# Kernel optimization log

Hardware: AMD Instinct MI355X
Metric: run time of the kernel (lower is better)

Reference implementation:

```python
import jax, jax.numpy as jnp
import numpy as np

H_PATCH, W_PATCH = 14, 14
NUM_HEADS, HEAD_DIM = 12, 64


def _relative_position_index(h, w):
    ch, cw = np.meshgrid(np.arange(h), np.arange(w), indexing='ij')
    coords = np.stack([ch.ravel(), cw.ravel()])          # (2, h*w)
    rel = coords[:, :, None] - coords[:, None, :]        # (2, L, L)
    rel = rel.transpose(1, 2, 0)
    rel[:, :, 0] += h - 1
    rel[:, :, 1] += w - 1
    rel[:, :, 0] *= 2 * w - 1
    return rel.sum(-1)                                    # (h*w, h*w) int


def setup_inputs() -> dict:
    key = jax.random.key(0)
    ks = jax.random.split(key, 16)
    B, L, C = 256, 197, 768
    s = 0.02
    return {
        'hidden_states': jax.random.normal(ks[0], (B, L, C), jnp.float32),
        'Wq': jax.random.normal(ks[1], (C, C), jnp.float32) * s,
        'bq': jax.random.normal(ks[2], (C,), jnp.float32) * s,
        'Wk': jax.random.normal(ks[3], (C, C), jnp.float32) * s,
        'bk': jax.random.normal(ks[4], (C,), jnp.float32) * s,
        'Wv': jax.random.normal(ks[5], (C, C), jnp.float32) * s,
        'bv': jax.random.normal(ks[6], (C,), jnp.float32) * s,
        'Wo': jax.random.normal(ks[7], (C, C), jnp.float32) * s,
        'bo': jax.random.normal(ks[8], (C,), jnp.float32) * s,
        'rel_table': jax.random.normal(ks[9], ((2 * H_PATCH - 1) * (2 * W_PATCH - 1), NUM_HEADS), jnp.float32) * s,
        'cls_to_patches': jax.random.normal(ks[10], (1, NUM_HEADS, 1, H_PATCH * W_PATCH), jnp.float32) * s,
        'patches_to_cls': jax.random.normal(ks[11], (1, NUM_HEADS, H_PATCH * W_PATCH, 1), jnp.float32) * s,
        'cls_to_cls': jax.random.normal(ks[12], (1, NUM_HEADS, 1, 1), jnp.float32) * s,
    }


def _full_bias(rel_table, cls_to_patches, patches_to_cls, cls_to_cls):
    idx = jnp.asarray(_relative_position_index(H_PATCH, W_PATCH))  # (P, P)
    patch_bias = rel_table[idx]                                    # (P, P, H)
    patch_bias = jnp.transpose(patch_bias, (2, 0, 1))[None]        # (1, H, P, P)
    top = jnp.concatenate([cls_to_cls, cls_to_patches], axis=-1)   # (1, H, 1, P+1)
    bottom = jnp.concatenate([patches_to_cls, patch_bias], axis=-1)
    return jnp.concatenate([top, bottom], axis=-2)                 # (1, H, L, L)


def reference(hidden_states, Wq, bq, Wk, bk, Wv, bv, Wo, bo,
              rel_table, cls_to_patches, patches_to_cls, cls_to_cls):
    B, L, C = hidden_states.shape
    Hh, D = NUM_HEADS, HEAD_DIM
    scale = D ** -0.5

    def heads(x, W, b):
        return (x @ W + b).reshape(B, L, Hh, D).transpose(0, 2, 1, 3)  # (B,H,L,D)

    q = heads(hidden_states, Wq, bq)
    k = heads(hidden_states, Wk, bk)
    v = heads(hidden_states, Wv, bv)

    attn = jnp.einsum('bhqd,bhkd->bhqk', q, k) * scale
    attn = attn + _full_bias(rel_table, cls_to_patches, patches_to_cls, cls_to_cls)
    attn = jax.nn.softmax(attn, axis=-1)

    x = jnp.einsum('bhqk,bhkd->bhqd', attn, v)            # (B,H,L,D)
    x = x.transpose(0, 2, 1, 3).reshape(B, L, C)
    return x @ Wo + bo
```

## Files before the change

kernel.cpp:

```cpp
#include <hip/hip_runtime.h>
#include <hip/hip_bf16.h>
#include <stdint.h>

#define LSEQ 197
#define NH   12
#define HD   64
#define CDIM 768
#define QKVS 2304

#define VSTRD 200

typedef __bf16 bf16x8 __attribute__((ext_vector_type(8)));
typedef float  f32x4  __attribute__((ext_vector_type(4)));
typedef unsigned short u16x4 __attribute__((ext_vector_type(4)));

__device__ __forceinline__ float bf2f(unsigned short u) { return __uint_as_float(((unsigned)u) << 16); }
__device__ __forceinline__ unsigned short f2bf(float f) {
  unsigned u = __float_as_uint(f);
  unsigned r = 0x7fffu + ((u >> 16) & 1u);
  return (unsigned short)((u + r) >> 16);
}

__device__ __forceinline__ void gload16(const void* g, void* l) {
  __builtin_amdgcn_global_load_lds(
      (const __attribute__((address_space(1))) unsigned int*)(g),
      (__attribute__((address_space(3))) unsigned int*)(l), 16, 0, 0);
}

__device__ __forceinline__ bf16x8 pack4(unsigned x, unsigned y, unsigned z, unsigned w) {
  union { unsigned u[4]; bf16x8 v; } t;
  t.u[0] = x; t.u[1] = y; t.u[2] = z; t.u[3] = w;
  return t.v;
}

__global__ void detect_dtype(const unsigned* __restrict__ x, int* __restrict__ flag) {
  __shared__ int cnt;
  if (threadIdx.x == 0) cnt = 0;
  __syncthreads();
  int local = 0;
  for (int i = threadIdx.x; i < 1024; i += 256) {
    const unsigned e = (x[i] >> 7) & 0xFFu;
    if (e >= 96u && e <= 140u) local++;
  }
  atomicAdd(&cnt, local);
  __syncthreads();
  if (threadIdx.x == 0) *flag = (cnt > 512) ? 0 : 1;
}

__global__ void convert_to_bf16(const void* __restrict__ in,
                                unsigned short* __restrict__ outb,
                                const int* __restrict__ flag, long n) {
  const long stride = (long)gridDim.x * blockDim.x;
  long i = (long)blockIdx.x * blockDim.x + threadIdx.x;
  if (*flag) {
    const float* f = (const float*)in;
    for (; i < n; i += stride) outb[i] = f2bf(f[i]);
  } else {
    const unsigned short* s = (const unsigned short*)in;
    for (; i < n; i += stride) outb[i] = s[i];
  }
}

__global__ void convert_small(const void* b0, const void* b1, const void* b2, const void* b3,
                              const void* r, const void* cp, const void* pc, const void* cc,
                              unsigned short* __restrict__ out, const int* __restrict__ flag) {
  const int starts[9] = {0, 768, 1536, 2304, 3072, 11820, 14172, 16524, 16536};
  const void* srcs[8] = {b0, b1, b2, b3, r, cp, pc, cc};
  const bool isf = (*flag != 0);
  for (int i = blockIdx.x * blockDim.x + threadIdx.x; i < 16536;
       i += gridDim.x * blockDim.x) {
    int seg = 0;
    while (i >= starts[seg + 1]) seg++;
    const int off = i - starts[seg];
    out[i] = isf ? f2bf(((const float*)srcs[seg])[off])
                 : ((const unsigned short*)srcs[seg])[off];
  }
}

__global__ void bias_build(const unsigned short* __restrict__ sm,
                           unsigned short* __restrict__ biasB) {
  const int gid = blockIdx.x * blockDim.x + threadIdx.x;
  if (gid >= 12 * 13 * 13 * 256) return;
  const int r    = gid & 3;
  const int lane = (gid >> 2) & 63;
  const int t    = gid >> 8;
  const int nt   = t % 13;
  const int mt   = (t / 13) % 13;
  const int h    = t / 169;
  const int q = mt * 16 + (lane & 15);
  const int k = nt * 16 + ((lane >> 4) & 3) * 4 + r;
  float v;
  if (q >= 197 || k >= 197) {
    v = -1e30f;
  } else {
    const unsigned short* rel = sm + 3072;
    const unsigned short* c2p = sm + 11820;
    const unsigned short* p2c = sm + 14172;
    const unsigned short* c2c = sm + 16524;
    unsigned short u;
    if (q == 0) {
      u = (k == 0) ? c2c[h] : c2p[h * 196 + (k - 1)];
    } else if (k == 0) {
      u = p2c[h * 196 + (q - 1)];
    } else {
      const int pi = q - 1, pj = k - 1;
      const int dh = pi / 14 - pj / 14 + 13;
      const int dw = pi % 14 - pj % 14 + 13;
      u = rel[(dh * 27 + dw) * 12 + h];
    }
    v = bf2f(u) * 1.4426950408889634f;
  }
  biasB[gid] = f2bf(v);
}

__global__ void transpose768_cvt(const void* __restrict__ in,
                                 unsigned short* __restrict__ out,
                                 const int* __restrict__ flag) {
  __shared__ unsigned short tile[32][33];
  const bool isf = (*flag != 0);
  const int tx = threadIdx.x & 31;
  const int ty = threadIdx.x >> 5;
  const int bx = blockIdx.x, by = blockIdx.y;
#pragma unroll
  for (int j = 0; j < 32; j += 8) {
    const size_t idx = (size_t)(by * 32 + ty + j) * CDIM + bx * 32 + tx;
    tile[ty + j][tx] = isf ? f2bf(((const float*)in)[idx])
                           : ((const unsigned short*)in)[idx];
  }
  __syncthreads();
#pragma unroll
  for (int j = 0; j < 32; j += 8)
    out[(size_t)(bx * 32 + ty + j) * CDIM + by * 32 + tx] = tile[tx][ty + j];
}

__global__ __launch_bounds__(256, 2) void gemm_bt_bias(
    const unsigned short* __restrict__ A,
    const unsigned short* __restrict__ Bt,
    const unsigned short* __restrict__ bias,
    void* __restrict__ C,
    int M, int N, int K,
    const int* __restrict__ outf32) {
  __shared__ unsigned short As[128 * 32];
  __shared__ unsigned short Bs[128 * 32];

  const int tid  = threadIdx.x;
  const int lane = tid & 63;
  const int wid  = tid >> 6;
  const int nwg = gridDim.x;
  const int q8 = nwg >> 3, r8 = nwg & 7;
  const int xcd = blockIdx.x & 7, ii = blockIdx.x >> 3;
  const int wg = (xcd < r8 ? xcd * (q8 + 1) : r8 * (q8 + 1) + (xcd - r8) * q8) + ii;
  const int nbn = N >> 7;
  const int bm = wg / nbn, bn = wg % nbn;
  const int wm = wid >> 1, wn = wid & 1;
  const bool wf32 = (outf32 != nullptr) && (*outf32 != 0);

  const int srow = (wid * 2) * 16 + (lane >> 2);
  const int scol = (lane & 3) * 8;
  const unsigned short* Ag = A  + (size_t)(bm * 128 + srow) * K + scol;
  const unsigned short* Bg = Bt + (size_t)(bn * 128 + srow) * K + scol;
  unsigned short* lA0 = &As[(wid * 2) * 16 * 32];
  unsigned short* lA1 = lA0 + 16 * 32;
  unsigned short* lB0 = &Bs[(wid * 2) * 16 * 32];
  unsigned short* lB1 = lB0 + 16 * 32;

  f32x4 acc[4][4] = {};

  for (int kt = 0; kt < K; kt += 32) {
    gload16(Ag, lA0);
    gload16(Ag + (size_t)16 * K, lA1);
    gload16(Bg, lB0);
    gload16(Bg + (size_t)16 * K, lB1);
    Ag += 32; Bg += 32;
    __syncthreads();

    bf16x8 fa[4], fb[4];
#pragma unroll
    for (int t = 0; t < 4; ++t) {
      fa[t] = *(const bf16x8*)&As[(wm * 64 + t * 16 + (lane & 15)) * 32 + (lane >> 4) * 8];
      fb[t] = *(const bf16x8*)&Bs[(wn * 64 + t * 16 + (lane & 15)) * 32 + (lane >> 4) * 8];
    }
#pragma unroll
    for (int mt = 0; mt < 4; ++mt)
#pragma unroll
      for (int nt = 0; nt < 4; ++nt)
        acc[mt][nt] = __builtin_amdgcn_mfma_f32_16x16x32_bf16(fa[mt], fb[nt], acc[mt][nt], 0, 0, 0);
    __syncthreads();
  }

  float bvv[4];
#pragma unroll
  for (int nt = 0; nt < 4; ++nt)
    bvv[nt] = bf2f(bias[bn * 128 + wn * 64 + nt * 16 + (lane & 15)]);

#pragma unroll
  for (int mt = 0; mt < 4; ++mt) {
    const int row0 = bm * 128 + wm * 64 + mt * 16 + (lane >> 4) * 4;
#pragma unroll
    for (int r = 0; r < 4; ++r) {
      const size_t rowoff = (size_t)(row0 + r) * N + bn * 128 + wn * 64 + (lane & 15);
#pragma unroll
      for (int nt = 0; nt < 4; ++nt) {
        const float val = acc[mt][nt][r] + bvv[nt];
        const size_t idx = rowoff + nt * 16;
        if (wf32) ((float*)C)[idx] = val;
        else      ((unsigned short*)C)[idx] = f2bf(val);
      }
    }
  }
}

__global__ __launch_bounds__(256, 3) void attn_mfma(
    const unsigned short* __restrict__ QKV,
    const unsigned short* __restrict__ biasB,
    unsigned short* __restrict__ ctx) {
  __shared__ unsigned short Kh[208 * 64];
  __shared__ unsigned short Vt[64 * VSTRD];

  const int tid  = threadIdx.x;
  const int lane = tid & 63;
  const int wid  = tid >> 6;
  const int bh = blockIdx.x;
  const int b = bh / NH;
  const int h = bh - b * NH;
  const size_t baseQ = (size_t)b * LSEQ * QKVS + (size_t)h * HD;
  const size_t baseK = baseQ + 768;
  const size_t baseV = baseQ + 1536;
  const size_t baseC = (size_t)b * LSEQ * CDIM + (size_t)h * HD;

  for (int i = tid; i < 197 * 8; i += 256) {
    const int l = i >> 3, c8 = (i & 7) * 8;
    const bf16x8 kv = *(const bf16x8*)&QKV[baseK + (size_t)l * QKVS + c8];
    *(bf16x8*)((char*)Kh + l * 128 + ((c8 * 2) ^ ((l & 7) << 4))) = kv;
  }
  for (int i = tid; i < 197 * 32; i += 256) {
    const int l = i >> 5, d2 = (i & 31) * 2;
    const unsigned vv = *(const unsigned*)&QKV[baseV + (size_t)l * QKVS + d2];
    Vt[d2 * VSTRD + l]       = (unsigned short)(vv & 0xffffu);
    Vt[(d2 + 1) * VSTRD + l] = (unsigned short)(vv >> 16);
  }
  for (int i = tid; i < 64 * 3; i += 256)
    Vt[(i / 3) * VSTRD + 197 + (i % 3)] = 0;
  __syncthreads();

  const int ql = lane & 15, g = lane >> 4;
  const int krd0 = ql * 128 + ((g * 16) ^ ((ql & 7) << 4));
  const int krd1 = ql * 128 + ((g * 16 + 64) ^ ((ql & 7) << 4));
  const int vrd  = ql * VSTRD + g * 8;
  const int vrd6 = ql * VSTRD + 192;
  const int addrA = (((g & 1) << 5) + ql) << 2;
  const int addrB = addrA + 64;
  const bool hi2 = lane >= 32;
  const bool hi1 = lane >= 16;

  for (int mt = wid; mt < 13; mt += 4) {
    const int qm = mt * 16 + ql;
    const unsigned short* qp =
        &QKV[baseQ + (size_t)(qm > 196 ? 196 : qm) * QKVS + g * 8];
    const bf16x8 qf0 = *(const bf16x8*)qp;
    const bf16x8 qf1 = *(const bf16x8*)(qp + 32);

    const unsigned short* bp =
        biasB + (size_t)(h * 13 + mt) * 13 * 256 + (lane << 2);
    u16x4 bq[13];
#pragma unroll
    for (int nt = 0; nt < 13; ++nt) bq[nt] = *(const u16x4*)(bp + nt * 256);

    f32x4 s[13];
#pragma unroll
    for (int nt = 0; nt < 13; ++nt) {
      const bf16x8 kb0 = *(const bf16x8*)((const char*)Kh + nt * 2048 + krd0);
      const bf16x8 kb1 = *(const bf16x8*)((const char*)Kh + nt * 2048 + krd1);
      f32x4 a = {0.f, 0.f, 0.f, 0.f};
      a = __builtin_amdgcn_mfma_f32_16x16x32_bf16(kb0, qf0, a, 0, 0, 0);
      a = __builtin_amdgcn_mfma_f32_16x16x32_bf16(kb1, qf1, a, 0, 0, 0);
      s[nt] = a;
    }

#pragma unroll
    for (int nt = 0; nt < 13; ++nt)
#pragma unroll
      for (int r = 0; r < 4; ++r)
        s[nt][r] = s[nt][r] * 0.18033688011112042f + bf2f(bq[nt][r]);

    const float NEG = -1e30f;
    s[12][0] = hi2 ? NEG : s[12][0];
    s[12][1] = hi1 ? NEG : s[12][1];
    s[12][2] = hi1 ? NEG : s[12][2];
    s[12][3] = hi1 ? NEG : s[12][3];

    float m0 = s[0][0], m1 = s[0][1], m2 = s[0][2], m3 = s[0][3];
#pragma unroll
    for (int nt = 1; nt < 13; ++nt) {
      m0 = fmaxf(m0, s[nt][0]); m1 = fmaxf(m1, s[nt][1]);
      m2 = fmaxf(m2, s[nt][2]); m3 = fmaxf(m3, s[nt][3]);
    }
    float m = fmaxf(fmaxf(m0, m1), fmaxf(m2, m3));
    m = fmaxf(m, __shfl_xor(m, 16));
    m = fmaxf(m, __shfl_xor(m, 32));
    float t0 = 0.f, t1 = 0.f, t2 = 0.f, t3 = 0.f;
#pragma unroll
    for (int nt = 0; nt < 13; ++nt) {
      s[nt][0] = __builtin_exp2f(s[nt][0] - m); t0 += s[nt][0];
      s[nt][1] = __builtin_exp2f(s[nt][1] - m); t1 += s[nt][1];
      s[nt][2] = __builtin_exp2f(s[nt][2] - m); t2 += s[nt][2];
      s[nt][3] = __builtin_exp2f(s[nt][3] - m); t3 += s[nt][3];
    }
    float sum = (t0 + t1) + (t2 + t3);
    sum += __shfl_xor(sum, 16);
    sum += __shfl_xor(sum, 32);
    const float inv = __builtin_amdgcn_rcpf(sum);

    unsigned pk0[13], pk1[13];
#pragma unroll
    for (int nt = 0; nt < 13; ++nt) {
      const float p0 = s[nt][0] * inv, p1 = s[nt][1] * inv;
      const float p2 = s[nt][2] * inv, p3 = s[nt][3] * inv;
      unsigned lo, hi;
      asm("v_cvt_pk_bf16_f32 %0, %1, %2" : "=v"(lo) : "v"(p0), "v"(p1));
      asm("v_cvt_pk_bf16_f32 %0, %1, %2" : "=v"(hi) : "v"(p2), "v"(p3));
      pk0[nt] = lo; pk1[nt] = hi;
    }

    f32x4 o[4] = {{0.f,0.f,0.f,0.f},{0.f,0.f,0.f,0.f},{0.f,0.f,0.f,0.f},{0.f,0.f,0.f,0.f}};
#pragma unroll
    for (int t = 0; t < 6; ++t) {
      const int i0 = 2 * t, i1 = 2 * t + 1;
      const int xA0 = __builtin_amdgcn_ds_bpermute(addrA, (int)pk0[i0]);
      const int yA0 = __builtin_amdgcn_ds_bpermute(addrA, (int)pk0[i1]);
      const int xA1 = __builtin_amdgcn_ds_bpermute(addrA, (int)pk1[i0]);
      const int yA1 = __builtin_amdgcn_ds_bpermute(addrA, (int)pk1[i1]);
      const int xB0 = __builtin_amdgcn_ds_bpermute(addrB, (int)pk0[i0]);
      const int yB0 = __builtin_amdgcn_ds_bpermute(addrB, (int)pk0[i1]);
      const int xB1 = __builtin_amdgcn_ds_bpermute(addrB, (int)pk1[i0]);
      const int yB1 = __builtin_amdgcn_ds_bpermute(addrB, (int)pk1[i1]);
      const bf16x8 pa = pack4((unsigned)(hi2 ? yA0 : xA0),
                              (unsigned)(hi2 ? yA1 : xA1),
                              (unsigned)(hi2 ? yB0 : xB0),
                              (unsigned)(hi2 ? yB1 : xB1));
#pragma unroll
      for (int ot = 0; ot < 4; ++ot) {
        const bf16x8 vbf = *(const bf16x8*)&Vt[ot * 16 * VSTRD + vrd + t * 32];
        o[ot] = __builtin_amdgcn_mfma_f32_16x16x32_bf16(pa, vbf, o[ot], 0, 0, 0);
      }
    }
    {
      const int xA0 = __builtin_amdgcn_ds_bpermute(addrA, (int)pk0[12]);
      const int xA1 = __builtin_amdgcn_ds_bpermute(addrA, (int)pk1[12]);
      const int xB0 = __builtin_amdgcn_ds_bpermute(addrB, (int)pk0[12]);
      const int xB1 = __builtin_amdgcn_ds_bpermute(addrB, (int)pk1[12]);
      const bf16x8 pa = pack4(hi2 ? 0u : (unsigned)xA0,
                              hi2 ? 0u : (unsigned)xA1,
                              hi2 ? 0u : (unsigned)xB0,
                              hi2 ? 0u : (unsigned)xB1);
#pragma unroll
      for (int ot = 0; ot < 4; ++ot) {
        const bf16x8 vbf = *(const bf16x8*)&Vt[ot * 16 * VSTRD + vrd6];
        o[ot] = __builtin_amdgcn_mfma_f32_16x16x32_bf16(pa, vbf, o[ot], 0, 0, 0);
      }
    }

#pragma unroll
    for (int r = 0; r < 4; ++r) {
      const int q = mt * 16 + g * 4 + r;
      if (q < LSEQ) {
#pragma unroll
        for (int ot = 0; ot < 4; ++ot)
          ctx[baseC + (size_t)q * CDIM + ot * 16 + ql] = f2bf(o[ot][r]);
      }
    }
  }
}

extern "C" void kernel_launch(void* const* d_in, const int* in_sizes, int n_in,
                              void* d_out, int out_size, void* d_ws, size_t ws_size,
                              hipStream_t stream) {
  const void* X   = d_in[0];
  const void* Wq  = d_in[1];
  const void* bq  = d_in[2];
  const void* Wk  = d_in[3];
  const void* bk  = d_in[4];
  const void* Wv  = d_in[5];
  const void* bv  = d_in[6];
  const void* Wo  = d_in[7];
  const void* bo  = d_in[8];
  const void* rel = d_in[9];
  const void* c2p = d_in[10];
  const void* p2c = d_in[11];
  const void* c2c = d_in[12];

  char* ws = (char*)d_ws;
  const size_t FLAG_OFF = 0;
  const size_t SM_OFF   = 256;
  const size_t BIAS_OFF = 40960;
  const size_t WT_OFF   = BIAS_OFF + 2080768;
  const size_t WT_SZ    = (size_t)CDIM * CDIM * 2;
  const size_t XB_OFF   = WT_OFF + 4 * WT_SZ;
  const size_t X_SZ     = (size_t)50432 * CDIM * 2;
  const size_t QKV_OFF  = XB_OFF + X_SZ;
  int* flag = (int*)(ws + FLAG_OFF);
  unsigned short* smb   = (unsigned short*)(ws + SM_OFF);
  unsigned short* biasB = (unsigned short*)(ws + BIAS_OFF);
  unsigned short* WqT = (unsigned short*)(ws + WT_OFF + 0 * WT_SZ);
  unsigned short* WkT = (unsigned short*)(ws + WT_OFF + 1 * WT_SZ);
  unsigned short* WvT = (unsigned short*)(ws + WT_OFF + 2 * WT_SZ);
  unsigned short* WoT = (unsigned short*)(ws + WT_OFF + 3 * WT_SZ);
  unsigned short* Xb  = (unsigned short*)(ws + XB_OFF);
  unsigned short* QKVb= (unsigned short*)(ws + QKV_OFF);
  unsigned short* Cb  = Xb;

  detect_dtype<<<1, 256, 0, stream>>>((const unsigned*)X, flag);

  convert_to_bf16<<<4096, 256, 0, stream>>>(X, Xb, flag, (long)50432 * CDIM);
  convert_small<<<65, 256, 0, stream>>>(bq, bk, bv, bo, rel, c2p, p2c, c2c, smb, flag);
  bias_build<<<2028, 256, 0, stream>>>(smb, biasB);

  dim3 tgrid(24, 24);
  transpose768_cvt<<<tgrid, 256, 0, stream>>>(Wq, WqT, flag);
  transpose768_cvt<<<tgrid, 256, 0, stream>>>(Wk, WkT, flag);
  transpose768_cvt<<<tgrid, 256, 0, stream>>>(Wv, WvT, flag);
  transpose768_cvt<<<tgrid, 256, 0, stream>>>(Wo, WoT, flag);

  gemm_bt_bias<<<dim3(18 * 394), 256, 0, stream>>>(Xb, WqT, smb, QKVb,
                                                   50432, QKVS, CDIM, nullptr);

  attn_mfma<<<dim3(256 * NH), 256, 0, stream>>>(QKVb, biasB, Cb);

  gemm_bt_bias<<<dim3(6 * 394), 256, 0, stream>>>(Cb, WoT, smb + 2304, d_out,
                                                  50432, CDIM, CDIM, flag);
}
```

Measured before the change: 856.8 us.

## Triple-buffer LDS tiles in GEMM to overlap global loads with MFMA

Turns the GEMM's single-buffered LDS tile loop into a three-stage ring buffer. Loads for tile t+2 are issued before tile t is computed, and explicit vmcnt waits plus barriers replace the two syncthreads per iteration. The goal is to hide global-to-LDS latency behind MFMA work and cut barriers from two to one per k-step. The cost is triple the LDS footprint (48KB per block), which may lower occupancy below the 2 blocks per CU in the launch bounds. It also relies on manual waitcnt correctness.

```diff
diff --git a/kernel.cpp b/kernel.cpp
--- a/kernel.cpp
+++ b/kernel.cpp
@@ -140,8 +140,8 @@
     void* __restrict__ C,
     int M, int N, int K,
     const int* __restrict__ outf32) {
-  __shared__ unsigned short As[128 * 32];
-  __shared__ unsigned short Bs[128 * 32];
+  __shared__ unsigned short As[3][128 * 32];
+  __shared__ unsigned short Bs[3][128 * 32];
 
   const int tid  = threadIdx.x;
   const int lane = tid & 63;
@@ -159,39 +159,55 @@
   const int scol = (lane & 3) * 8;
   const unsigned short* Ag = A  + (size_t)(bm * 128 + srow) * K + scol;
   const unsigned short* Bg = Bt + (size_t)(bn * 128 + srow) * K + scol;
-  unsigned short* lA0 = &As[(wid * 2) * 16 * 32];
-  unsigned short* lA1 = lA0 + 16 * 32;
-  unsigned short* lB0 = &Bs[(wid * 2) * 16 * 32];
-  unsigned short* lB1 = lB0 + 16 * 32;
+  const int swave = (wid * 2) * 16 * 32;
 
   f32x4 acc[4][4] = {};
-
-  for (int kt = 0; kt < K; kt += 32) {
-    gload16(Ag, lA0);
-    gload16(Ag + (size_t)16 * K, lA1);
-    gload16(Bg, lB0);
-    gload16(Bg + (size_t)16 * K, lB1);
-    Ag += 32; Bg += 32;
-    __syncthreads();
-
-    bf16x8 fa[4], fb[4];
-#pragma unroll
-    for (int t = 0; t < 4; ++t) {
-      fa[t] = *(const bf16x8*)&As[(wm * 64 + t * 16 + (lane & 15)) * 32 + (lane >> 4) * 8];
-      fb[t] = *(const bf16x8*)&Bs[(wn * 64 + t * 16 + (lane & 15)) * 32 + (lane >> 4) * 8];
-    }
-#pragma unroll
-    for (int mt = 0; mt < 4; ++mt)
-#pragma unroll
-      for (int nt = 0; nt < 4; ++nt)
-        acc[mt][nt] = __builtin_amdgcn_mfma_f32_16x16x32_bf16(fa[mt], fb[nt], acc[mt][nt], 0, 0, 0);
-    __syncthreads();
-  }
+  const int nt = K >> 5;
+
+#define STAGE(bufi) do {                                         \
+    gload16(Ag, &As[bufi][swave]);                               \
+    gload16(Ag + (size_t)16 * K, &As[bufi][swave + 512]);        \
+    gload16(Bg, &Bs[bufi][swave]);                               \
+    gload16(Bg + (size_t)16 * K, &Bs[bufi][swave + 512]);        \
+    Ag += 32; Bg += 32; } while (0)
+
+#define COMPUTE(bufi) do {                                                         \
+    bf16x8 fa[4], fb[4];                                                           \
+    _Pragma("unroll")                                                              \
+    for (int t4 = 0; t4 < 4; ++t4) {                                               \
+      fa[t4] = *(const bf16x8*)&As[bufi][(wm * 64 + t4 * 16 + (lane & 15)) * 32 + (lane >> 4) * 8]; \
+      fb[t4] = *(const bf16x8*)&Bs[bufi][(wn * 64 + t4 * 16 + (lane & 15)) * 32 + (lane >> 4) * 8]; \
+    }                                                                              \
+    _Pragma("unroll")                                                              \
+    for (int mt = 0; mt < 4; ++mt)                                                 \
+      _Pragma("unroll")                                                            \
+      for (int ntt = 0; ntt < 4; ++ntt)                                            \
+        acc[mt][ntt] = __builtin_amdgcn_mfma_f32_16x16x32_bf16(fa[mt], fb[ntt], acc[mt][ntt], 0, 0, 0); \
+    } while (0)
+
+  STAGE(0);
+  STAGE(1);
+  asm volatile("s_waitcnt vmcnt(4)" ::: "memory");
+  __builtin_amdgcn_s_barrier();
+
+#pragma unroll 3
+  for (int t = 0; t < nt; ++t) {
+    if (t + 2 < nt) STAGE((t + 2) % 3);
+    __builtin_amdgcn_sched_barrier(0);
+    COMPUTE(t % 3);
+    if (t + 1 < nt) {
+      if (t + 2 < nt) asm volatile("s_waitcnt vmcnt(4)" ::: "memory");
+      else            asm volatile("s_waitcnt vmcnt(0)" ::: "memory");
+      __builtin_amdgcn_s_barrier();
+    }
+  }
+#undef STAGE
+#undef COMPUTE
 
   float bvv[4];
 #pragma unroll
-  for (int nt = 0; nt < 4; ++nt)
-    bvv[nt] = bf2f(bias[bn * 128 + wn * 64 + nt * 16 + (lane & 15)]);
+  for (int c = 0; c < 4; ++c)
+    bvv[c] = bf2f(bias[bn * 128 + wn * 64 + c * 16 + (lane & 15)]);
 
 #pragma unroll
   for (int mt = 0; mt < 4; ++mt) {
@@ -200,9 +216,9 @@
     for (int r = 0; r < 4; ++r) {
       const size_t rowoff = (size_t)(row0 + r) * N + bn * 128 + wn * 64 + (lane & 15);
 #pragma unroll
-      for (int nt = 0; nt < 4; ++nt) {
-        const float val = acc[mt][nt][r] + bvv[nt];
-        const size_t idx = rowoff + nt * 16;
+      for (int c = 0; c < 4; ++c) {
+        const float val = acc[mt][c][r] + bvv[c];
+        const size_t idx = rowoff + c * 16;
         if (wf32) ((float*)C)[idx] = val;
         else      ((unsigned short*)C)[idx] = f2bf(val);
       }
```

Measured after the change: 895.7 us. +4.5%, slower.
